# Performance work log

Hardware: AMD Instinct MI355X
Metric: run time of the kernel (lower is better)

The kernel has to match this reference:

```python
import jax, jax.numpy as jnp
import numpy as np

N_BINS = 18
EPS = 1e-9


def setup_inputs() -> dict:
    key = jax.random.key(0)
    k1, k2 = jax.random.split(key)
    # pha: phase values in [-pi, pi], shape (B, C, Fp, S, T)
    pha = jax.random.uniform(k1, (4, 16, 10, 4, 2048), dtype=jnp.float32,
                             minval=-np.pi, maxval=np.pi)
    # amp: non-negative amplitude envelope, shape (B, C, Fa, S, T)
    amp = jax.random.uniform(k2, (4, 16, 30, 4, 2048), dtype=jnp.float32)
    return {"pha": pha, "amp": amp}


def reference(pha, amp):
    # Bin cutoffs: linspace(-pi, pi, n_bins+1), matching the torch buffer.
    cutoffs = jnp.linspace(-np.pi, np.pi, N_BINS + 1, dtype=jnp.float32)
    # torch.bucketize(right=False) == searchsorted side='left'; then -1, clamp.
    bins = jnp.clip(jnp.searchsorted(cutoffs, pha, side='left') - 1, 0, N_BINS - 1)
    # One-hot mask over phase bins: (B, C, Fp, S, T, K)
    onehot = jax.nn.one_hot(bins, N_BINS, dtype=amp.dtype)
    # Per-bin amplitude sums, contracting over time t (avoids the torch 7D tensor):
    # amp_sums[b,c,p,a,s,k] = sum_t onehot[b,c,p,s,t,k] * amp[b,c,a,s,t]
    amp_sums = jnp.einsum('bcpstk,bcast->bcpask', onehot, amp)  # (B,C,Fp,Fa,S,K)
    counts = onehot.sum(axis=4)  # (B, C, Fp, S, K)
    amp_means = amp_sums / (counts[:, :, :, None] + EPS)  # broadcast over Fa
    amp_probs = amp_means / (amp_means.sum(axis=-1, keepdims=True) + EPS)
    # Negative entropy term over bins: (B, C, Fp, Fa, S)
    ent = (amp_probs * jnp.log(amp_probs + EPS)).sum(axis=-1)
    MI = (jnp.log(N_BINS + EPS) + ent) / jnp.log(jnp.float32(N_BINS))
    # Mean over segments -> (B, C, Fp, Fa)
    return MI.mean(axis=-1)
```

## Files before the change

### kernel.cpp

```cpp
#include <hip/hip_runtime.h>
#include <math.h>


#define FP_ 10
#define FA_ 30
#define K_  18
#define T_  2048
#define TC_ 256
#define NTILE 8
#define NT_ 512

#define OFF_BINS 128
#define BINROW   2064
#define BSW_     516
#define OFF_LO   (OFF_BINS + FP_ * BINROW)
#define PROW     272
#define PLSZ     (32 * PROW)
#define OFF_HI   (OFF_LO + PLSZ)
#define LDS_TOTAL (OFF_HI + PLSZ)
#define OFF_RED  128
#define OFF_CNT  25472

typedef int i32x4 __attribute__((ext_vector_type(4)));

static __device__ __forceinline__ unsigned oh8(unsigned w, unsigned kb4) {
  const unsigned x = w ^ kb4;
  const unsigned t = (x & 0x7F7F7F7Fu) + 0x7F7F7F7Fu;
  return ((~(t | x)) & 0x80808080u) >> 7;
}

__global__ __launch_bounds__(NT_, 2)
void mi_main(const float* __restrict__ pha, const float* __restrict__ amp,
             float* __restrict__ out) {
  extern __shared__ unsigned char smem[];
  float*    c_lds = (float*)smem;
  unsigned* binsw = (unsigned*)(smem + OFF_BINS);
  float*    red   = (float*)(smem + OFF_RED);
  int*      cnt_t = (int*)(smem + OFF_CNT);

  const int tid  = threadIdx.x;
  const int lane = tid & 63;
  const int wv   = tid >> 6;
  const int quad = lane >> 4;
  const int lc   = lane & 15;
  const int mq   = wv & 3;
  const int q2   = wv >> 2;

  const int g  = blockIdx.x;
  const int s  = g & 3;
  const int bc = g >> 2;
  const long pha_base = (long)bc * (FP_ * 4L * T_) + (long)s * T_;
  const long amp_base = (long)bc * (FA_ * 4L * T_) + (long)s * T_;

  if (tid < 19) {
    const double PI_D = 3.14159265358979323846264338327950288;
    const double step = (2.0 * PI_D) / 18.0;
    c_lds[tid] = (tid == 18) ? (float)PI_D : (float)(-PI_D + (double)tid * step);
  }
  if (tid < 17) {
    *(uint4*)(smem + OFF_LO + 30 * PROW + tid * 16) =
        make_uint4(0x01010101u, 0x01010101u, 0x01010101u, 0x01010101u);
    *(uint4*)(smem + OFF_LO + 31 * PROW + tid * 16) = make_uint4(0u, 0u, 0u, 0u);
    *(uint4*)(smem + OFF_HI + 30 * PROW + tid * 16) = make_uint4(0u, 0u, 0u, 0u);
    *(uint4*)(smem + OFF_HI + 31 * PROW + tid * 16) = make_uint4(0u, 0u, 0u, 0u);
  }

  const bool stager = tid < 480;
  const int a_row = tid >> 4;
  const int seg   = tid & 15;
  const float* gsrc = amp + amp_base + (long)a_row * (4L * T_) + seg * 16;
  float4 vreg[4];
  if (stager) {
    #pragma unroll
    for (int j = 0; j < 4; ++j) vreg[j] = *(const float4*)(gsrc + j * 4);
  }

  const float PI_F    = 3.14159274101257324f;
  const float INVSTEP = 2.8647890f;
  #pragma unroll 2
  for (int p = 0; p < FP_; ++p) {
    const float4 v = *(const float4*)(pha + pha_base + (long)p * (4L * T_) + tid * 4);
    const float xs[4] = {v.x, v.y, v.z, v.w};
    unsigned pk = 0;
    #pragma unroll
    for (int j = 0; j < 4; ++j) {
      const float x = xs[j];
      int gi = (int)((x + PI_F) * INVSTEP);
      gi = min(17, max(0, gi));
      if (x <= c_lds[gi]) gi -= 1;
      else if (x > c_lds[gi + 1]) gi += 1;
      gi = min(17, max(0, gi));
      pk |= ((unsigned)gi) << (8 * j);
    }
    binsw[p * BSW_ + tid] = pk;
  }

  int p_mt[3]; unsigned kb4_mt[3];
  #pragma unroll
  for (int mt = 0; mt < 3; ++mt) {
    const int row = mq * 48 + mt * 16 + lc;
    int p = row / 18; p = min(p, 9);
    const unsigned kb = (unsigned)(row - p * 18);
    p_mt[mt] = p;
    kb4_mt[mt] = kb * 0x01010101u;
  }

  i32x4 accl[3][2], acch[3][2];
  #pragma unroll
  for (int mt = 0; mt < 3; ++mt) {
    accl[mt][0] = (i32x4){0,0,0,0}; accl[mt][1] = (i32x4){0,0,0,0};
    acch[mt][0] = (i32x4){0,0,0,0}; acch[mt][1] = (i32x4){0,0,0,0};
  }
  __syncthreads();

  #pragma unroll 1
  for (int tile = 0; tile < NTILE; ++tile) {
    if (stager) {
      unsigned lo[4], hi[4];
      #pragma unroll
      for (int j = 0; j < 4; ++j) {
        const float xv[4] = {vreg[j].x, vreg[j].y, vreg[j].z, vreg[j].w};
        unsigned q[4];
        #pragma unroll
        for (int e = 0; e < 4; ++e)
          q[e] = min((unsigned)(xv[e] * 65536.0f), 65535u);
        const unsigned w01 = q[0] | (q[1] << 16);
        const unsigned w23 = q[2] | (q[3] << 16);
        lo[j] = __builtin_amdgcn_perm(w23, w01, 0x06040200u) ^ 0x80808080u;
        hi[j] = __builtin_amdgcn_perm(w23, w01, 0x07050301u) ^ 0x80808080u;
      }
      *(uint4*)(smem + OFF_LO + a_row * PROW + seg * 16) = make_uint4(lo[0], lo[1], lo[2], lo[3]);
      *(uint4*)(smem + OFF_HI + a_row * PROW + seg * 16) = make_uint4(hi[0], hi[1], hi[2], hi[3]);
    }
    __syncthreads();
    if (stager && tile < NTILE - 1) {
      #pragma unroll
      for (int j = 0; j < 4; ++j)
        vreg[j] = *(const float4*)(gsrc + (tile + 1) * TC_ + j * 4);
    }

    #pragma unroll
    for (int ci = 0; ci < 2; ++ci) {
      const int cl = q2 * 2 + ci;
      const unsigned char* bl = smem + OFF_LO + cl * 64 + quad * 16;
      const unsigned char* bh = smem + OFF_HI + cl * 64 + quad * 16;
      const i32x4 Bl0 = *(const i32x4*)(bl + lc * PROW);
      const i32x4 Bl1 = *(const i32x4*)(bl + (16 + lc) * PROW);
      const i32x4 Bh0 = *(const i32x4*)(bh + lc * PROW);
      const i32x4 Bh1 = *(const i32x4*)(bh + (16 + lc) * PROW);
      const int chg = tile * 4 + cl;
      #pragma unroll
      for (int mt = 0; mt < 3; ++mt) {
        const uint4 wb = *(const uint4*)(smem + OFF_BINS + p_mt[mt] * BINROW
                                         + chg * 64 + quad * 16);
        const unsigned kb4 = kb4_mt[mt];
        const i32x4 A = (i32x4){(int)oh8(wb.x, kb4), (int)oh8(wb.y, kb4),
                                (int)oh8(wb.z, kb4), (int)oh8(wb.w, kb4)};
        accl[mt][0] = __builtin_amdgcn_mfma_i32_16x16x64_i8(A, Bl0, accl[mt][0], 0, 0, 0);
        acch[mt][0] = __builtin_amdgcn_mfma_i32_16x16x64_i8(A, Bh0, acch[mt][0], 0, 0, 0);
        accl[mt][1] = __builtin_amdgcn_mfma_i32_16x16x64_i8(A, Bl1, accl[mt][1], 0, 0, 0);
        acch[mt][1] = __builtin_amdgcn_mfma_i32_16x16x64_i8(A, Bh1, acch[mt][1], 0, 0, 0);
      }
    }
    __syncthreads();
  }

  if (lc == 14) {
    #pragma unroll
    for (int mt = 0; mt < 3; ++mt)
      #pragma unroll
      for (int r = 0; r < 4; ++r)
        cnt_t[q2 * 192 + mq * 48 + mt * 16 + quad * 4 + r] = accl[mt][1][r];
  }
  __syncthreads();

  float vals[3][2][4];
  #pragma unroll
  for (int mt = 0; mt < 3; ++mt)
    #pragma unroll
    for (int n = 0; n < 2; ++n)
      #pragma unroll
      for (int r = 0; r < 4; ++r) {
        const int row = mq * 48 + mt * 16 + quad * 4 + r;
        const int cnt = cnt_t[q2 * 192 + row];
        const int raw = (acch[mt][n][r] << 8) + accl[mt][n][r] + 32896 * cnt;
        float v = (float)raw * 1.52587890625e-5f;
        if (n == 1 && lc == 14) v = (float)accl[mt][n][r];
        vals[mt][n][r] = v;
      }
  __syncthreads();

  if (q2 == 1) {
    float* S = &red[mq * 48 * 33];
    #pragma unroll
    for (int mt = 0; mt < 3; ++mt)
      #pragma unroll
      for (int n = 0; n < 2; ++n)
        #pragma unroll
        for (int r = 0; r < 4; ++r)
          S[(mt * 16 + quad * 4 + r) * 33 + n * 16 + lc] = vals[mt][n][r];
  }
  __syncthreads();
  if (q2 == 0) {
    float* S = &red[mq * 48 * 33];
    #pragma unroll
    for (int mt = 0; mt < 3; ++mt)
      #pragma unroll
      for (int n = 0; n < 2; ++n)
        #pragma unroll
        for (int r = 0; r < 4; ++r) {
          const int idx = (mt * 16 + quad * 4 + r) * 33 + n * 16 + lc;
          S[idx] = vals[mt][n][r] + S[idx];
        }
  }
  __syncthreads();

  if (tid < FP_ * FA_) {
    const int p = tid / FA_;
    const int a = tid - p * FA_;
    float m[K_];
    float tot = 0.0f;
    #pragma unroll
    for (int k = 0; k < K_; ++k) {
      const float cnt = red[(p * K_ + k) * 33 + 30];
      const float sv  = red[(p * K_ + k) * 33 + a];
      const float mk  = sv / (cnt + 1e-9f);
      m[k] = mk;
      tot += mk;
    }
    const float denom = tot + 1e-9f;
    float ent = 0.0f;
    #pragma unroll
    for (int k = 0; k < K_; ++k) {
      const float pr = m[k] / denom;
      ent += pr * logf(pr + 1e-9f);
    }
    const float L  = logf(18.0f);
    const float mi = (L + ent) / L;
    atomicAdd(&out[(bc * FP_ + p) * FA_ + a], 0.25f * mi);
  }
}

extern "C" void kernel_launch(void* const* d_in, const int* in_sizes, int n_in,
                              void* d_out, int out_size, void* d_ws, size_t ws_size,
                              hipStream_t stream) {
  const float* pha = (const float*)d_in[0];
  const float* amp = (const float*)d_in[1];
  float* out = (float*)d_out;

  hipMemsetAsync(d_out, 0, (size_t)out_size * sizeof(float), stream);
  hipLaunchKernelGGL(mi_main, dim3(256), dim3(NT_), LDS_TOTAL, stream, pha, amp, out);
}
```

Measured before the change: 116.0 us.

## Split time axis across two blocks with workspace partial reduction

Each (b,c,s) group is now handled by two blocks, each covering half of the time axis, so the grid doubles from 256 to 512 blocks and occupancy is raised to 4 blocks per CU. Each block writes its reduced per-bin sums and counts to a global workspace slot. An atomic ticket picks the second-arriving block, which adds its partner's partials and computes the entropy/MI epilogue. This is meant to fill more CUs on the MI355X, at the cost of extra global traffic, a second memset and a fence-plus-atomic handshake.

```diff
diff --git a/kernel.cpp b/kernel.cpp
--- a/kernel.cpp
+++ b/kernel.cpp
@@ -6,13 +6,14 @@
 #define FA_ 30
 #define K_  18
 #define T_  2048
+#define TH_ 1024
 #define TC_ 256
-#define NTILE 8
+#define NTILE 4
 #define NT_ 512
 
 #define OFF_BINS 128
-#define BINROW   2064
-#define BSW_     516
+#define BINROW   1040
+#define BSW_     260
 #define OFF_LO   (OFF_BINS + FP_ * BINROW)
 #define PROW     272
 #define PLSZ     (32 * PROW)
@@ -21,6 +22,9 @@
 #define OFF_RED  128
 #define OFF_CNT  25472
 
+#define SLOT_    6336
+#define CNT_OFF  (512 * SLOT_)
+
 typedef int i32x4 __attribute__((ext_vector_type(4)));
 
 static __device__ __forceinline__ unsigned oh8(unsigned w, unsigned kb4) {
@@ -29,10 +33,11 @@
   return ((~(t | x)) & 0x80808080u) >> 7;
 }
 
-__global__ __launch_bounds__(NT_, 2)
+__global__ __launch_bounds__(NT_, 4)
 void mi_main(const float* __restrict__ pha, const float* __restrict__ amp,
-             float* __restrict__ out) {
+             float* __restrict__ ws, float* __restrict__ out) {
   extern __shared__ unsigned char smem[];
+  __shared__ unsigned ticket_lds;
   float*    c_lds = (float*)smem;
   unsigned* binsw = (unsigned*)(smem + OFF_BINS);
   float*    red   = (float*)(smem + OFF_RED);
@@ -46,11 +51,13 @@
   const int mq   = wv & 3;
   const int q2   = wv >> 2;
 
-  const int g  = blockIdx.x;
-  const int s  = g & 3;
-  const int bc = g >> 2;
-  const long pha_base = (long)bc * (FP_ * 4L * T_) + (long)s * T_;
-  const long amp_base = (long)bc * (FA_ * 4L * T_) + (long)s * T_;
+  const int bid  = blockIdx.x;
+  const int g    = bid >> 1;
+  const int half = bid & 1;
+  const int s    = g & 3;
+  const int bc   = g >> 2;
+  const long pha_base = (long)bc * (FP_ * 4L * T_) + (long)s * T_ + half * TH_;
+  const long amp_base = (long)bc * (FA_ * 4L * T_) + (long)s * T_ + half * TH_;
 
   if (tid < 19) {
     const double PI_D = 3.14159265358979323846264338327950288;
@@ -77,9 +84,11 @@
 
   const float PI_F    = 3.14159274101257324f;
   const float INVSTEP = 2.8647890f;
-  #pragma unroll 2
-  for (int p = 0; p < FP_; ++p) {
-    const float4 v = *(const float4*)(pha + pha_base + (long)p * (4L * T_) + tid * 4);
+  #pragma unroll
+  for (int it = 0; it < 5; ++it) {
+    const int i = it * NT_ + tid;
+    const int p = i >> 8, w = i & 255;
+    const float4 v = *(const float4*)(pha + pha_base + (long)p * (4L * T_) + w * 4);
     const float xs[4] = {v.x, v.y, v.z, v.w};
     unsigned pk = 0;
     #pragma unroll
@@ -92,7 +101,7 @@
       gi = min(17, max(0, gi));
       pk |= ((unsigned)gi) << (8 * j);
     }
-    binsw[p * BSW_ + tid] = pk;
+    binsw[p * BSW_ + w] = pk;
   }
 
   int p_mt[3]; unsigned kb4_mt[3];
@@ -215,6 +224,31 @@
   }
   __syncthreads();
 
+  float* slot = ws + (long)bid * SLOT_;
+  #pragma unroll
+  for (int it = 0; it < 13; ++it) {
+    const int i = it * NT_ + tid;
+    if (i < SLOT_) slot[i] = red[i];
+  }
+  __syncthreads();
+  if (tid == 0) {
+    __threadfence();
+    unsigned* cnt = (unsigned*)(ws + CNT_OFF);
+    ticket_lds = __hip_atomic_fetch_add(&cnt[g], 1u, __ATOMIC_ACQ_REL,
+                                        __HIP_MEMORY_SCOPE_AGENT);
+  }
+  __syncthreads();
+  if (ticket_lds == 0) return;
+
+  __threadfence();
+  const float* partner = ws + (long)(bid ^ 1) * SLOT_;
+  #pragma unroll
+  for (int it = 0; it < 13; ++it) {
+    const int i = it * NT_ + tid;
+    if (i < SLOT_) red[i] += partner[i];
+  }
+  __syncthreads();
+
   if (tid < FP_ * FA_) {
     const int p = tid / FA_;
     const int a = tid - p * FA_;
@@ -247,7 +281,10 @@
   const float* pha = (const float*)d_in[0];
   const float* amp = (const float*)d_in[1];
   float* out = (float*)d_out;
+  float* ws  = (float*)d_ws;
 
   hipMemsetAsync(d_out, 0, (size_t)out_size * sizeof(float), stream);
-  hipLaunchKernelGGL(mi_main, dim3(256), dim3(NT_), LDS_TOTAL, stream, pha, amp, out);
+  hipMemsetAsync((char*)d_ws + (size_t)CNT_OFF * 4, 0, 256 * 4, stream);
+  hipLaunchKernelGGL(mi_main, dim3(512), dim3(NT_), LDS_TOTAL, stream,
+                     pha, amp, ws, out);
 }
```

New measurement: 214.2 us. 1.85x slower.
